# Performance work log

Measured on AMD Instinct MI355X. Metric: run time of the kernel, lower is better.

Reference implementation:

```python
import jax, jax.numpy as jnp
import numpy as np
from jax import lax

STRIDE = 2
PAD = 2
K = 5

def conv_transpose3d(x, w, b):
    # x: (N, Cin, D, H, W); w: (Cin, Cout, kD, kH, kW) torch layout
    # Equivalent dense conv: flip kernel spatially, swap in/out, lhs-dilate by stride,
    # pad each side by (K - 1 - PAD).
    w_t = jnp.flip(w, axis=(2, 3, 4)).transpose(1, 0, 2, 3, 4)  # (Cout, Cin, kD, kH, kW)
    p = K - 1 - PAD  # = 2
    y = lax.conv_general_dilated(
        x, w_t,
        window_strides=(1, 1, 1),
        padding=[(p, p)] * 3,
        lhs_dilation=(STRIDE,) * 3,
        dimension_numbers=('NCDHW', 'OIDHW', 'NCDHW'))
    return y + b[None, :, None, None, None]

def maxpool3d(x, k):
    return lax.reduce_window(
        x, -jnp.inf, lax.max,
        window_dimensions=(1, 1, k, k, k),
        window_strides=(1, 1, k, k, k),
        padding='VALID')

def setup_inputs() -> dict:
    key = jax.random.key(0)
    k1, k2, k3 = jax.random.split(key, 3)
    x = jax.random.normal(k1, (16, 32, 16, 32, 32), dtype=jnp.float32)
    weight = jax.random.normal(k2, (32, 64, 5, 5, 5), dtype=jnp.float32) * 0.05
    bias = jax.random.normal(k3, (64,), dtype=jnp.float32) * 0.05
    return {"x": x, "weight": weight, "bias": bias}

def reference(x, weight, bias):
    y = conv_transpose3d(x, weight, bias)      # (16, 64, 31, 63, 63)
    y = maxpool3d(y, 2)                        # (16, 64, 15, 31, 31)
    y = maxpool3d(y, 3)                        # (16, 64, 5, 10, 10)
    return jnp.sum(y, axis=1, keepdims=True)   # (16, 1, 5, 10, 10)
```

## Files before the change

### kernel.cpp

```cpp
#include <hip/hip_runtime.h>

typedef short v8s __attribute__((ext_vector_type(8)));
typedef float v4f __attribute__((ext_vector_type(4)));

#define N_  16
#define CI_ 32
#define CO_ 64
#define DI  16
#define HI  32
#define WI  32
#define NEGINF (-__builtin_inff())

__device__ __forceinline__ unsigned short f2bf(float f) {
    unsigned int u = __float_as_uint(f);
    unsigned int r = (u + 0x7FFFu + ((u >> 16) & 1u)) >> 16;
    return (unsigned short)r;
}

__device__ __forceinline__ void gld16(const void* g, void* l) {
    __builtin_amdgcn_global_load_lds(
        (const __attribute__((address_space(1))) void*)g,
        (__attribute__((address_space(3))) void*)l, 16, 0, 0);
}

__constant__ int O64c[9] = {0, 55296, 92160, 129024, 153600, 190464, 215040, 239616, 256000};

__global__ void prep(const float* __restrict__ x, const float* __restrict__ w,
                     unsigned short* __restrict__ xp, unsigned short* __restrict__ wt,
                     float* __restrict__ out, int do_x) {
    if (blockIdx.x < 1088) {
        if (!do_x) return;
        __shared__ __align__(16) unsigned short tl[8192];
        const int bi = blockIdx.x;
        const int pd = bi % 17;
        const int cg = (bi / 17) & 3;
        const int n  = bi / 68;
        if (pd > 0) {
            const int c = threadIdx.x >> 5;
            const int ww = threadIdx.x & 31;
            const float* xc = x + (((size_t)(n * 32 + cg * 8 + c) * 16 + (pd - 1)) * 32) * 32;
            #pragma unroll
            for (int h = 0; h < 32; ++h)
                tl[(h * 32 + ww) * 8 + c] = f2bf(xc[h * 32 + ww]);
        }
        __syncthreads();
        unsigned short* xpo = xp + (size_t)bi * 8448;
        for (int o = threadIdx.x; o < 1056; o += 256) {
            int ph = o / 33, pw = o - ph * 33;
            v8s v;
            if (pd == 0 || ph == 0 || pw == 0) v = (v8s){0, 0, 0, 0, 0, 0, 0, 0};
            else v = *(const v8s*)&tl[((ph - 1) * 32 + pw - 1) * 8];
            *(v8s*)(xpo + o * 8) = v;
        }
    } else {
        if (blockIdx.x == 1088 && threadIdx.x < 64) {
            int tb = 1536 + threadIdx.x;
            int whalf = tb & 1, hj = (tb >> 1) % 10, dj = (tb / 20) % 5, n = tb / 100;
            float* o = out + (((size_t)(n * 5 + dj) * 10 + hj) * 10 + whalf * 5);
            #pragma unroll
            for (int j = 0; j < 5; ++j) o[j] = 0.f;
        }
        int u = (blockIdx.x - 1088) * 256 + threadIdx.x;
        if (u >= 256000) return;
        int r = 0;
        #pragma unroll
        for (int i = 1; i < 8; ++i) r += (u >= O64c[i]);
        const int rd = r >> 2, rh = (r >> 1) & 1, rw = r & 1;
        const int nh = rh ? 2 : 3, nw = rw ? 2 : 3;
        int t2 = u - O64c[r];
        int j   = t2 & 7;
        int l   = (t2 >> 3) & 15;
        int q   = (t2 >> 7) & 3;
        int nt  = (t2 >> 9) & 3;
        int tap = t2 >> 11;
        int co = nt * 16 + l;
        int ci = q * 8 + j;
        int jw = tap % nw;
        int jh = (tap / nw) % nh;
        int jd = tap / (nw * nh);
        int kd = rd + 2 * jd, kh = rh + 2 * jh, kw = rw + 2 * jw;
        wt[u] = f2bf(w[(ci * CO_ + co) * 125 + kd * 25 + kh * 5 + kw]);
    }
}

__device__ __forceinline__ void run_class_f(
        const unsigned short* __restrict__ xs,
        int laneAB,
        const unsigned short* __restrict__ wcls,
        const int taps, const int nw, const int nh,
        unsigned Bm, bool isQ3, float (&pmax)[4][2])
{
    const char* xb = (const char*)xs;

    v4f acc[9][4];
    #pragma unroll
    for (int t = 0; t < 9; ++t)
        #pragma unroll
        for (int nt = 0; nt < 4; ++nt)
            acc[t][nt] = (v4f){0.f, 0.f, 0.f, 0.f};

    v8s B0[4], B1[4];
    #pragma unroll
    for (int nt = 0; nt < 4; ++nt) B0[nt] = *(const v8s*)(wcls + nt * 512);

    int aoff = 0, jw = 0, jh = 0;
    auto adv = [&]() {
        aoff += 16; ++jw;
        if (jw == nw) { jw = 0; aoff += 288 - 16 * nw; ++jh;
            if (jh == nh) { jh = 0; aoff += 1440 - 288 * nh; } }
    };
    auto comp = [&](const v8s (&B)[4]) {
        const int va = laneAB - aoff;
        static constexpr int RO[9] = {0, 576, 1728, 2880, 3456, 288, 1440, 2016, 3168};
        #pragma unroll
        for (int rr = 0; rr < 9; ++rr) {
            v8s a = *(const v8s*)(xb + va + RO[rr]);
            #pragma unroll
            for (int nt = 0; nt < 4; ++nt)
                acc[rr][nt] = __builtin_amdgcn_mfma_f32_16x16x32_bf16(a, B[nt], acc[rr][nt], 0, 0, 0);
        }
    };

    int s = 0;
    while (s + 2 <= taps) {
        #pragma unroll
        for (int nt = 0; nt < 4; ++nt)
            B1[nt] = *(const v8s*)(wcls + ((s + 1) * 4 + nt) * 512);
        comp(B0); adv();
        if (s + 2 < taps) {
            #pragma unroll
            for (int nt = 0; nt < 4; ++nt)
                B0[nt] = *(const v8s*)(wcls + ((s + 2) * 4 + nt) * 512);
        }
        comp(B1); adv();
        s += 2;
    }
    if (s < taps) comp(B0);

    #pragma unroll
    for (int nt = 0; nt < 4; ++nt) {
        #pragma unroll
        for (int reg = 0; reg < 4; ++reg) {
            float v = acc[0][nt][reg];
            #pragma unroll
            for (int rr = 1; rr < 9; ++rr) v = fmaxf(v, acc[rr][nt][reg]);
            if (reg == 3) v = isQ3 ? NEGINF : v;
            const bool bB = (Bm >> reg) & 1u;
            pmax[nt][0] = fmaxf(pmax[nt][0], bB ? NEGINF : v);
            pmax[nt][1] = fmaxf(pmax[nt][1], bB ? v : NEGINF);
        }
    }
}

__device__ __forceinline__ void run_class_t(
        const unsigned short* __restrict__ xs,
        int laneAB,
        const unsigned short* __restrict__ wcls,
        const int taps, const int nw, const int nh,
        unsigned Bm, bool isQ3, float (&pmax)[2])
{
    const char* xb = (const char*)xs;

    v4f acc[9];
    #pragma unroll
    for (int t = 0; t < 9; ++t) acc[t] = (v4f){0.f, 0.f, 0.f, 0.f};

    v8s B0 = *(const v8s*)(wcls);
    v8s B1;

    int aoff = 0, jw = 0, jh = 0;
    auto adv = [&]() {
        aoff += 16; ++jw;
        if (jw == nw) { jw = 0; aoff += 288 - 16 * nw; ++jh;
            if (jh == nh) { jh = 0; aoff += 1440 - 288 * nh; } }
    };
    auto comp = [&](v8s B) {
        const int va = laneAB - aoff;
        static constexpr int RO[9] = {0, 576, 1728, 2880, 3456, 288, 1440, 2016, 3168};
        #pragma unroll
        for (int rr = 0; rr < 9; ++rr) {
            v8s a = *(const v8s*)(xb + va + RO[rr]);
            acc[rr] = __builtin_amdgcn_mfma_f32_16x16x32_bf16(a, B, acc[rr], 0, 0, 0);
        }
    };

    int s = 0;
    while (s + 2 <= taps) {
        B1 = *(const v8s*)(wcls + (s + 1) * 2048);
        comp(B0); adv();
        if (s + 2 < taps) B0 = *(const v8s*)(wcls + (s + 2) * 2048);
        comp(B1); adv();
        s += 2;
    }
    if (s < taps) comp(B0);

    #pragma unroll
    for (int reg = 0; reg < 4; ++reg) {
        float v = acc[0][reg];
        #pragma unroll
        for (int rr = 1; rr < 9; ++rr) v = fmaxf(v, acc[rr][reg]);
        if (reg == 3) v = isQ3 ? NEGINF : v;
        const bool bB = (Bm >> reg) & 1u;
        pmax[0] = fmaxf(pmax[0], bB ? NEGINF : v);
        pmax[1] = fmaxf(pmax[1], bB ? v : NEGINF);
    }
}

template<bool PRE>
__global__ __launch_bounds__(256, 2)
void fused_main(const float* __restrict__ x, const unsigned short* __restrict__ xp,
                const unsigned short* __restrict__ wt,
                const float* __restrict__ bias, float* __restrict__ out) {
    __shared__ __align__(16) char smem[28800];
    unsigned short* xs = (unsigned short*)smem;
    float* P = (float*)smem;
    float* Y = (float*)(smem + 9472);

    const int b = blockIdx.x;
    const bool tail = (b >= 1536);
    int tile, sub;
    if (tail) { int u = b - 1536; tile = 1536 + (u >> 2); sub = u & 3; }
    else      { tile = b; sub = 0; }

    const int whalf = tile & 1;
    const int hj = (tile >> 1) % 10;
    const int dj = (tile / 20) % 5;
    const int n  = tile / 100;

    const int lane = threadIdx.x & 63;
    const int wv   = threadIdx.x >> 6;

    if (PRE) {
        const int t = threadIdx.x;
        #pragma unroll
        for (int i = 0; i < 8; ++i) {
            int c = i * 256 + t;
            if (c < 1800) {
                int row = c / 18;
                int iwc = c - row * 18;
                int cg  = row / 25;
                int rr  = row - cg * 25;
                int idl = rr / 5;
                int ihl = rr - idl * 5;
                size_t goff = ((((size_t)((n * 4 + cg) * 17 + 3 * dj + idl)) * 32
                                + 3 * hj + ihl) * 33 + 15 * whalf + iwc) * 8;
                gld16(xp + goff, smem + i * 4096 + wv * 1024);
            }
        }
    } else {
        const int id0 = 3 * dj - 1, ih0 = 3 * hj - 1, iwb = 15 * whalf - 1;
        const float* xn = x + (size_t)n * (CI_ * DI * HI * WI);
        for (int e = threadIdx.x; e < 14400; e += 256) {
            int ci   = e / 450;
            int rem  = e - ci * 450;
            int idp  = rem / 90;
            int rem2 = rem - idp * 90;
            int ihp  = rem2 / 18;
            int iwp  = rem2 - ihp * 18;
            int id = id0 + idp, ih = ih0 + ihp, iw = iwb + iwp;
            float v = 0.f;
            if (id >= 0 && ih >= 0 && iw >= 0)
                v = xn[((ci * DI + id) * HI + ih) * WI + iw];
            xs[(ci >> 3) * 3600 + idp * 720 + ihp * 144 + iwp * 8 + (ci & 7)] = f2bf(v);
        }
    }
    __syncthreads();

    const int l = lane & 15, q = lane >> 4;
    const int laneAB = q * 7200 + (l + 2) * 16 + 3456;

    static constexpr int tapsT[8] = {27, 18, 18, 12, 18, 12, 12, 8};
    static constexpr int O64[8]   = {0, 55296, 92160, 129024, 153600, 190464, 215040, 239616};
    static constexpr int nwT[8]   = {3, 2, 3, 2, 3, 2, 3, 2};
    static constexpr int nhT[8]   = {3, 3, 2, 2, 3, 3, 2, 2};
    static constexpr int uOff[5] = {0, 2, 4, 6, 8};
    static constexpr int uR[8]   = {0, 7,  1, 3,  2, 5,  4, 6};

    static constexpr int wjAt[4] = {0, 1, 2, 4};
    static constexpr int wjBt[4] = {1, 2, 3, 5};

    const unsigned Bm = (0x0EC8u >> (q << 2)) & 0xFu;
    const bool isQ3 = (q == 3);
    const int u0 = uOff[wv], u1 = uOff[wv + 1];

    if (!tail) {
        float pmax[4][2];
        #pragma unroll
        for (int nt = 0; nt < 4; ++nt) { pmax[nt][0] = NEGINF; pmax[nt][1] = NEGINF; }

        #pragma unroll 1
        for (int iu = u0; iu < u1; ++iu) {
            const int r = uR[iu];
            run_class_f(xs, laneAB, wt + O64[r] + lane * 8,
                        tapsT[r], nwT[r], nhT[r], Bm, isQ3, pmax);
        }

        __syncthreads();
        {
            int base = ((wv * 4 + q) * 16 + l) * 9;
            #pragma unroll
            for (int nt = 0; nt < 4; ++nt) {
                P[base + nt * 2 + 0] = pmax[nt][0];
                P[base + nt * 2 + 1] = pmax[nt][1];
            }
        }
        __syncthreads();

        for (int oi = threadIdx.x; oi < 320; oi += 256) {
            int co = oi / 5;
            int wjl = oi - co * 5;
            int lc = co & 15, ntc = co >> 4;
            float v = NEGINF;
            #pragma unroll
            for (int w = 0; w < 4; ++w) {
                #pragma unroll
                for (int qq = 0; qq < 4; ++qq) {
                    const float* pp = &P[((w * 4 + qq) * 16 + lc) * 9 + ntc * 2];
                    if (wjAt[qq] == wjl) v = fmaxf(v, pp[0]);
                    if (wjBt[qq] == wjl) v = fmaxf(v, pp[1]);
                }
            }
            Y[co * 5 + wjl] = v + bias[co];
        }
        __syncthreads();

        if (wv == 0) {
            float vy[5];
            #pragma unroll
            for (int wjl = 0; wjl < 5; ++wjl) vy[wjl] = Y[lane * 5 + wjl];
            #pragma unroll
            for (int wjl = 0; wjl < 5; ++wjl) {
                float v = vy[wjl];
                #pragma unroll
                for (int off = 32; off > 0; off >>= 1)
                    v += __shfl_down(v, off, 64);
                if (lane == 0)
                    out[((n * 5 + dj) * 10 + hj) * 10 + whalf * 5 + wjl] = v;
            }
        }
    } else {
        float pmax1[2];
        pmax1[0] = NEGINF; pmax1[1] = NEGINF;

        #pragma unroll 1
        for (int iu = u0; iu < u1; ++iu) {
            const int r = uR[iu];
            run_class_t(xs, laneAB, wt + O64[r] + sub * 512 + lane * 8,
                        tapsT[r], nwT[r], nhT[r], Bm, isQ3, pmax1);
        }

        __syncthreads();
        {
            int base = ((wv * 4 + q) * 16 + l) * 9;
            P[base + sub * 2 + 0] = pmax1[0];
            P[base + sub * 2 + 1] = pmax1[1];
        }
        __syncthreads();

        if (wv == 0) {
            const int co = lane;
            const int lc = co & 15, ntc = co >> 4;
            const bool valid = (ntc == sub);
            float vy[5];
            #pragma unroll
            for (int wjl = 0; wjl < 5; ++wjl) vy[wjl] = NEGINF;
            #pragma unroll
            for (int w = 0; w < 4; ++w) {
                #pragma unroll
                for (int qq = 0; qq < 4; ++qq) {
                    const float* pp = &P[((w * 4 + qq) * 16 + lc) * 9 + sub * 2];
                    float a = pp[0], bv = pp[1];
                    #pragma unroll
                    for (int wjl = 0; wjl < 5; ++wjl) {
                        if (wjAt[qq] == wjl) vy[wjl] = fmaxf(vy[wjl], a);
                        if (wjBt[qq] == wjl) vy[wjl] = fmaxf(vy[wjl], bv);
                    }
                }
            }
            #pragma unroll
            for (int wjl = 0; wjl < 5; ++wjl) {
                float v = valid ? (vy[wjl] + bias[co]) : 0.f;
                #pragma unroll
                for (int off = 32; off > 0; off >>= 1)
                    v += __shfl_down(v, off, 64);
                if (lane == 0)
                    atomicAdd(&out[((n * 5 + dj) * 10 + hj) * 10 + whalf * 5 + wjl], v);
            }
        }
    }
}

extern "C" void kernel_launch(void* const* d_in, const int* in_sizes, int n_in,
                              void* d_out, int out_size, void* d_ws, size_t ws_size,
                              hipStream_t stream) {
    const float* x    = (const float*)d_in[0];
    const float* w    = (const float*)d_in[1];
    const float* bias = (const float*)d_in[2];
    float*       out  = (float*)d_out;
    unsigned short* wt = (unsigned short*)d_ws;
    unsigned short* xp = (unsigned short*)((char*)d_ws + 512512);
    const size_t XP_NEED = 512512 + 18382848;
    const int do_x = (ws_size >= XP_NEED) ? 1 : 0;

    prep<<<dim3(2088), 256, 0, stream>>>(x, w, xp, wt, out, do_x);
    if (do_x)
        fused_main<true ><<<dim3(1792), 256, 0, stream>>>(x, xp, wt, bias, out);
    else
        fused_main<false><<<dim3(1792), 256, 0, stream>>>(x, xp, wt, bias, out);
}
```

Before: 174.6 us.

## Merge prep and main kernels into one persistent cooperative kernel with grid sync

Replaces the two-launch sequence (prep then fused_main) with one cooperative kernel of 512 persistent blocks. The blocks first do the input/weight bf16 repacking, then pass a grid-wide barrier and loop over the conv/pool tiles. The aim is to remove the second launch and its inter-kernel gap. In exchange, the tile work is now scheduled statically: 3 full tiles per block plus a tail that lands on half the blocks, which leaves the load imbalanced. The tile body moves into a noinline device function, which may add call overhead or cost register allocation quality.

```diff
diff --git a/kernel.cpp b/kernel.cpp
--- a/kernel.cpp
+++ b/kernel.cpp
@@ -1,4 +1,5 @@
 #include <hip/hip_runtime.h>
+#include <hip/hip_cooperative_groups.h>
 
 typedef short v8s __attribute__((ext_vector_type(8)));
 typedef float v4f __attribute__((ext_vector_type(4)));
@@ -25,61 +26,74 @@
 
 __constant__ int O64c[9] = {0, 55296, 92160, 129024, 153600, 190464, 215040, 239616, 256000};
 
+
+__device__ __forceinline__ void xprep_block(int bi, const float* __restrict__ x,
+                                            unsigned short* __restrict__ xp,
+                                            unsigned short* tl) {
+    const int pd = bi % 17;
+    const int cg = (bi / 17) & 3;
+    const int n  = bi / 68;
+    if (pd > 0) {
+        const int c = threadIdx.x >> 5;
+        const int ww = threadIdx.x & 31;
+        const float* xc = x + (((size_t)(n * 32 + cg * 8 + c) * 16 + (pd - 1)) * 32) * 32;
+        #pragma unroll
+        for (int h = 0; h < 32; ++h)
+            tl[(h * 32 + ww) * 8 + c] = f2bf(xc[h * 32 + ww]);
+    }
+    __syncthreads();
+    unsigned short* xpo = xp + (size_t)bi * 8448;
+    for (int o = threadIdx.x; o < 1056; o += 256) {
+        int ph = o / 33, pw = o - ph * 33;
+        v8s v;
+        if (pd == 0 || ph == 0 || pw == 0) v = (v8s){0, 0, 0, 0, 0, 0, 0, 0};
+        else v = *(const v8s*)&tl[((ph - 1) * 32 + pw - 1) * 8];
+        *(v8s*)(xpo + o * 8) = v;
+    }
+}
+
+__device__ __forceinline__ void wprep_one(int u, const float* __restrict__ w,
+                                          unsigned short* __restrict__ wt) {
+    int r = 0;
+    #pragma unroll
+    for (int i = 1; i < 8; ++i) r += (u >= O64c[i]);
+    const int rd = r >> 2, rh = (r >> 1) & 1, rw = r & 1;
+    const int nh = rh ? 2 : 3, nw = rw ? 2 : 3;
+    int t2 = u - O64c[r];
+    int j   = t2 & 7;
+    int l   = (t2 >> 3) & 15;
+    int q   = (t2 >> 7) & 3;
+    int nt  = (t2 >> 9) & 3;
+    int tap = t2 >> 11;
+    int co = nt * 16 + l;
+    int ci = q * 8 + j;
+    int jw = tap % nw;
+    int jh = (tap / nw) % nh;
+    int jd = tap / (nw * nh);
+    int kd = rd + 2 * jd, kh = rh + 2 * jh, kw = rw + 2 * jw;
+    wt[u] = f2bf(w[(ci * CO_ + co) * 125 + kd * 25 + kh * 5 + kw]);
+}
+
+__device__ __forceinline__ void tailzero(float* __restrict__ out, int t) {
+    int tb = 1536 + t;
+    int whalf = tb & 1, hj = (tb >> 1) % 10, dj = (tb / 20) % 5, n = tb / 100;
+    float* o = out + (((size_t)(n * 5 + dj) * 10 + hj) * 10 + whalf * 5);
+    #pragma unroll
+    for (int j = 0; j < 5; ++j) o[j] = 0.f;
+}
+
 __global__ void prep(const float* __restrict__ x, const float* __restrict__ w,
                      unsigned short* __restrict__ xp, unsigned short* __restrict__ wt,
                      float* __restrict__ out, int do_x) {
     if (blockIdx.x < 1088) {
         if (!do_x) return;
         __shared__ __align__(16) unsigned short tl[8192];
-        const int bi = blockIdx.x;
-        const int pd = bi % 17;
-        const int cg = (bi / 17) & 3;
-        const int n  = bi / 68;
-        if (pd > 0) {
-            const int c = threadIdx.x >> 5;
-            const int ww = threadIdx.x & 31;
-            const float* xc = x + (((size_t)(n * 32 + cg * 8 + c) * 16 + (pd - 1)) * 32) * 32;
-            #pragma unroll
-            for (int h = 0; h < 32; ++h)
-                tl[(h * 32 + ww) * 8 + c] = f2bf(xc[h * 32 + ww]);
-        }
-        __syncthreads();
-        unsigned short* xpo = xp + (size_t)bi * 8448;
-        for (int o = threadIdx.x; o < 1056; o += 256) {
-            int ph = o / 33, pw = o - ph * 33;
-            v8s v;
-            if (pd == 0 || ph == 0 || pw == 0) v = (v8s){0, 0, 0, 0, 0, 0, 0, 0};
-            else v = *(const v8s*)&tl[((ph - 1) * 32 + pw - 1) * 8];
-            *(v8s*)(xpo + o * 8) = v;
-        }
+        xprep_block(blockIdx.x, x, xp, tl);
     } else {
-        if (blockIdx.x == 1088 && threadIdx.x < 64) {
-            int tb = 1536 + threadIdx.x;
-            int whalf = tb & 1, hj = (tb >> 1) % 10, dj = (tb / 20) % 5, n = tb / 100;
-            float* o = out + (((size_t)(n * 5 + dj) * 10 + hj) * 10 + whalf * 5);
-            #pragma unroll
-            for (int j = 0; j < 5; ++j) o[j] = 0.f;
-        }
+        if (blockIdx.x == 1088 && threadIdx.x < 64) tailzero(out, threadIdx.x);
         int u = (blockIdx.x - 1088) * 256 + threadIdx.x;
         if (u >= 256000) return;
-        int r = 0;
-        #pragma unroll
-        for (int i = 1; i < 8; ++i) r += (u >= O64c[i]);
-        const int rd = r >> 2, rh = (r >> 1) & 1, rw = r & 1;
-        const int nh = rh ? 2 : 3, nw = rw ? 2 : 3;
-        int t2 = u - O64c[r];
-        int j   = t2 & 7;
-        int l   = (t2 >> 3) & 15;
-        int q   = (t2 >> 7) & 3;
-        int nt  = (t2 >> 9) & 3;
-        int tap = t2 >> 11;
-        int co = nt * 16 + l;
-        int ci = q * 8 + j;
-        int jw = tap % nw;
-        int jh = (tap / nw) % nh;
-        int jd = tap / (nw * nh);
-        int kd = rd + 2 * jd, kh = rh + 2 * jh, kw = rw + 2 * jw;
-        wt[u] = f2bf(w[(ci * CO_ + co) * 125 + kd * 25 + kh * 5 + kw]);
+        wprep_one(u, w, wt);
     }
 }
 
@@ -207,20 +221,14 @@
 }
 
 template<bool PRE>
-__global__ __launch_bounds__(256, 2)
-void fused_main(const float* __restrict__ x, const unsigned short* __restrict__ xp,
-                const unsigned short* __restrict__ wt,
-                const float* __restrict__ bias, float* __restrict__ out) {
-    __shared__ __align__(16) char smem[28800];
+__device__ __attribute__((noinline)) void do_tile(
+        int tile, int sub, bool tail,
+        const float* __restrict__ x, const unsigned short* __restrict__ xp,
+        const unsigned short* __restrict__ wt, const float* __restrict__ bias,
+        float* __restrict__ out, char* smem) {
     unsigned short* xs = (unsigned short*)smem;
     float* P = (float*)smem;
     float* Y = (float*)(smem + 9472);
-
-    const int b = blockIdx.x;
-    const bool tail = (b >= 1536);
-    int tile, sub;
-    if (tail) { int u = b - 1536; tile = 1536 + (u >> 2); sub = u & 3; }
-    else      { tile = b; sub = 0; }
 
     const int whalf = tile & 1;
     const int hj = (tile >> 1) % 10;
@@ -388,6 +396,49 @@
             }
         }
     }
+    __syncthreads();
+}
+
+template<bool PRE>
+__global__ __launch_bounds__(256, 2)
+void fused_main(const float* __restrict__ x, const unsigned short* __restrict__ xp,
+                const unsigned short* __restrict__ wt,
+                const float* __restrict__ bias, float* __restrict__ out) {
+    __shared__ __align__(16) char smem[28800];
+    const int b = blockIdx.x;
+    const bool tail = (b >= 1536);
+    int tile, sub;
+    if (tail) { int u = b - 1536; tile = 1536 + (u >> 2); sub = u & 3; }
+    else      { tile = b; sub = 0; }
+    do_tile<PRE>(tile, sub, tail, x, xp, wt, bias, out, smem);
+}
+
+__global__ __launch_bounds__(256, 2)
+void mono(const float* __restrict__ x, const float* __restrict__ w,
+          const float* __restrict__ bias, unsigned short* __restrict__ xp,
+          unsigned short* __restrict__ wt, float* __restrict__ out) {
+    __shared__ __align__(16) char smem[28800];
+
+    #pragma unroll 1
+    for (int bi = blockIdx.x; bi < 1088; bi += 512) {
+        xprep_block(bi, x, xp, (unsigned short*)smem);
+        __syncthreads();
+    }
+    #pragma unroll 1
+    for (int u = blockIdx.x * 256 + threadIdx.x; u < 256000; u += 512 * 256)
+        wprep_one(u, w, wt);
+    if (blockIdx.x == 511 && threadIdx.x < 64) tailzero(out, threadIdx.x);
+
+    __threadfence();
+    cooperative_groups::this_grid().sync();
+
+    #pragma unroll 1
+    for (int rep = 0; rep < 3; ++rep)
+        do_tile<true>((int)blockIdx.x + rep * 512, 0, false, x, xp, wt, bias, out, smem);
+    if (blockIdx.x >= 256) {
+        int qb = blockIdx.x - 256;
+        do_tile<true>(1536 + (qb >> 2), qb & 3, true, x, xp, wt, bias, out, smem);
+    }
 }
 
 extern "C" void kernel_launch(void* const* d_in, const int* in_sizes, int n_in,
@@ -402,9 +453,17 @@
     const size_t XP_NEED = 512512 + 18382848;
     const int do_x = (ws_size >= XP_NEED) ? 1 : 0;
 
-    prep<<<dim3(2088), 256, 0, stream>>>(x, w, xp, wt, out, do_x);
-    if (do_x)
+    if (do_x) {
+        void* args[6] = {(void*)&x, (void*)&w, (void*)&bias,
+                         (void*)&xp, (void*)&wt, (void*)&out};
+        hipError_t e = hipLaunchCooperativeKernel((const void*)mono, dim3(512),
+                                                  dim3(256), args, 0, stream);
+        if (e == hipSuccess) return;
+        (void)hipGetLastError();
+        prep<<<dim3(2088), 256, 0, stream>>>(x, w, xp, wt, out, 1);
         fused_main<true ><<<dim3(1792), 256, 0, stream>>>(x, xp, wt, bias, out);
-    else
+    } else {
+        prep<<<dim3(2088), 256, 0, stream>>>(x, w, xp, wt, out, 0);
         fused_main<false><<<dim3(1792), 256, 0, stream>>>(x, xp, wt, bias, out);
-}
+    }
+}
```

Result: slower. 314.2 us (+79.9%).

## Split output-channel tiles into two halves to cut accumulator registers and raise occupancy

Applied to the files above, without the earlier changes.

The main conv-pool loop now processes the 64 output channels in two passes of 32 (two 16-wide MFMA tiles each) instead of all four tiles at once. This halves the accumulator array from 36 to 18 v4f registers, and the launch bound goes from 2 to 3 blocks per CU to exploit the lower register pressure. In exchange, every input A fragment is read from LDS twice per class, and the tap loop and pool reduction run twice, adding LDS traffic and loop overhead.

```diff
diff --git a/kernel.cpp b/kernel.cpp
--- a/kernel.cpp
+++ b/kernel.cpp
@@ -83,25 +83,28 @@
     }
 }
 
-__device__ __forceinline__ void run_class_f(
+__device__ __forceinline__ void run_class_h(
         const unsigned short* __restrict__ xs,
         int laneAB,
-        const unsigned short* __restrict__ wcls,
+        const unsigned short* __restrict__ wclsh,
         const int taps, const int nw, const int nh,
-        unsigned Bm, bool isQ3, float (&pmax)[4][2])
+        unsigned Bm, bool isQ3, float (&pm)[2][2])
 {
     const char* xb = (const char*)xs;
 
-    v4f acc[9][4];
+    v4f acc[9][2];
     #pragma unroll
-    for (int t = 0; t < 9; ++t)
-        #pragma unroll
-        for (int nt = 0; nt < 4; ++nt)
-            acc[t][nt] = (v4f){0.f, 0.f, 0.f, 0.f};
-
-    v8s B0[4], B1[4];
-    #pragma unroll
-    for (int nt = 0; nt < 4; ++nt) B0[nt] = *(const v8s*)(wcls + nt * 512);
+    for (int t = 0; t < 9; ++t) {
+        acc[t][0] = (v4f){0.f, 0.f, 0.f, 0.f};
+        acc[t][1] = (v4f){0.f, 0.f, 0.f, 0.f};
+    }
+
+    v8s P0[2], P1[2], P2[2], P3[2];
+    P0[0] = *(const v8s*)(wclsh + 0);
+    P0[1] = *(const v8s*)(wclsh + 512);
+    P1[0] = *(const v8s*)(wclsh + 2048);
+    P1[1] = *(const v8s*)(wclsh + 2048 + 512);
+    P2[0] = P0[0]; P2[1] = P0[1]; P3[0] = P1[0]; P3[1] = P1[1];
 
     int aoff = 0, jw = 0, jh = 0;
     auto adv = [&]() {
@@ -109,45 +112,46 @@
         if (jw == nw) { jw = 0; aoff += 288 - 16 * nw; ++jh;
             if (jh == nh) { jh = 0; aoff += 1440 - 288 * nh; } }
     };
-    auto comp = [&](const v8s (&B)[4]) {
+    auto comp = [&](const v8s (&B)[2]) {
         const int va = laneAB - aoff;
         static constexpr int RO[9] = {0, 576, 1728, 2880, 3456, 288, 1440, 2016, 3168};
         #pragma unroll
         for (int rr = 0; rr < 9; ++rr) {
             v8s a = *(const v8s*)(xb + va + RO[rr]);
-            #pragma unroll
-            for (int nt = 0; nt < 4; ++nt)
-                acc[rr][nt] = __builtin_amdgcn_mfma_f32_16x16x32_bf16(a, B[nt], acc[rr][nt], 0, 0, 0);
+            acc[rr][0] = __builtin_amdgcn_mfma_f32_16x16x32_bf16(a, B[0], acc[rr][0], 0, 0, 0);
+            acc[rr][1] = __builtin_amdgcn_mfma_f32_16x16x32_bf16(a, B[1], acc[rr][1], 0, 0, 0);
         }
     };
 
     int s = 0;
     while (s + 2 <= taps) {
-        #pragma unroll
-        for (int nt = 0; nt < 4; ++nt)
-            B1[nt] = *(const v8s*)(wcls + ((s + 1) * 4 + nt) * 512);
-        comp(B0); adv();
         if (s + 2 < taps) {
-            #pragma unroll
-            for (int nt = 0; nt < 4; ++nt)
-                B0[nt] = *(const v8s*)(wcls + ((s + 2) * 4 + nt) * 512);
-        }
-        comp(B1); adv();
+            P2[0] = *(const v8s*)(wclsh + (s + 2) * 2048);
+            P2[1] = *(const v8s*)(wclsh + (s + 2) * 2048 + 512);
+        }
+        if (s + 3 < taps) {
+            P3[0] = *(const v8s*)(wclsh + (s + 3) * 2048);
+            P3[1] = *(const v8s*)(wclsh + (s + 3) * 2048 + 512);
+        }
+        comp(P0); adv();
+        comp(P1); adv();
+        P0[0] = P2[0]; P0[1] = P2[1];
+        P1[0] = P3[0]; P1[1] = P3[1];
         s += 2;
     }
-    if (s < taps) comp(B0);
+    if (s < taps) comp(P0);
 
     #pragma unroll
-    for (int nt = 0; nt < 4; ++nt) {
+    for (int j = 0; j < 2; ++j) {
         #pragma unroll
         for (int reg = 0; reg < 4; ++reg) {
-            float v = acc[0][nt][reg];
-            #pragma unroll
-            for (int rr = 1; rr < 9; ++rr) v = fmaxf(v, acc[rr][nt][reg]);
+            float v = acc[0][j][reg];
+            #pragma unroll
+            for (int rr = 1; rr < 9; ++rr) v = fmaxf(v, acc[rr][j][reg]);
             if (reg == 3) v = isQ3 ? NEGINF : v;
             const bool bB = (Bm >> reg) & 1u;
-            pmax[nt][0] = fmaxf(pmax[nt][0], bB ? NEGINF : v);
-            pmax[nt][1] = fmaxf(pmax[nt][1], bB ? v : NEGINF);
+            pm[j][0] = fmaxf(pm[j][0], bB ? NEGINF : v);
+            pm[j][1] = fmaxf(pm[j][1], bB ? v : NEGINF);
         }
     }
 }
@@ -207,7 +211,7 @@
 }
 
 template<bool PRE>
-__global__ __launch_bounds__(256, 2)
+__global__ __launch_bounds__(256, 3)
 void fused_main(const float* __restrict__ x, const unsigned short* __restrict__ xp,
                 const unsigned short* __restrict__ wt,
                 const float* __restrict__ bias, float* __restrict__ out) {
@@ -291,8 +295,23 @@
         #pragma unroll 1
         for (int iu = u0; iu < u1; ++iu) {
             const int r = uR[iu];
-            run_class_f(xs, laneAB, wt + O64[r] + lane * 8,
-                        tapsT[r], nwT[r], nhT[r], Bm, isQ3, pmax);
+            #pragma unroll 1
+            for (int h = 0; h < 2; ++h) {
+                float pm[2][2] = {{NEGINF, NEGINF}, {NEGINF, NEGINF}};
+                run_class_h(xs, laneAB, wt + O64[r] + h * 1024 + lane * 8,
+                            tapsT[r], nwT[r], nhT[r], Bm, isQ3, pm);
+                if (h == 0) {
+                    pmax[0][0] = fmaxf(pmax[0][0], pm[0][0]);
+                    pmax[0][1] = fmaxf(pmax[0][1], pm[0][1]);
+                    pmax[1][0] = fmaxf(pmax[1][0], pm[1][0]);
+                    pmax[1][1] = fmaxf(pmax[1][1], pm[1][1]);
+                } else {
+                    pmax[2][0] = fmaxf(pmax[2][0], pm[0][0]);
+                    pmax[2][1] = fmaxf(pmax[2][1], pm[0][1]);
+                    pmax[3][0] = fmaxf(pmax[3][0], pm[1][0]);
+                    pmax[3][1] = fmaxf(pmax[3][1], pm[1][1]);
+                }
+            }
         }
 
         __syncthreads();
```

New measurement: 179.9 us. 1.03x slower.

## Switch conv MFMA tiles from 16x16x32 to 32x32x16 bf16 with repacked weights

Applied to the files above, without the earlier changes.

The implicit-GEMM convolution now uses 32x32x16 bf16 MFMA instead of 16x16x32. The weight prep packing, the A-operand addressing (two ci halves per lane group), the accumulator-to-pool masking and the LDS partial-max layout are all reworked to match the 32x32 output fragment. The aim is fewer MFMA issues and fewer LDS A-loads per tap. The tail blocks now split Cout into 2 halves instead of 4, giving a smaller grid, and setprio is raised around the MFMA bursts. Risks are higher register pressure from the 16-wide accumulators and subtle indexing errors in the remapped layouts.

```diff
diff --git a/kernel.cpp b/kernel.cpp
--- a/kernel.cpp
+++ b/kernel.cpp
@@ -1,7 +1,7 @@
 #include <hip/hip_runtime.h>
 
 typedef short v8s __attribute__((ext_vector_type(8)));
-typedef float v4f __attribute__((ext_vector_type(4)));
+typedef float v16f __attribute__((ext_vector_type(16)));
 
 #define N_  16
 #define CI_ 32
@@ -67,14 +67,14 @@
         for (int i = 1; i < 8; ++i) r += (u >= O64c[i]);
         const int rd = r >> 2, rh = (r >> 1) & 1, rw = r & 1;
         const int nh = rh ? 2 : 3, nw = rw ? 2 : 3;
-        int t2 = u - O64c[r];
-        int j   = t2 & 7;
-        int l   = (t2 >> 3) & 15;
-        int q   = (t2 >> 7) & 3;
-        int nt  = (t2 >> 9) & 3;
-        int tap = t2 >> 11;
-        int co = nt * 16 + l;
-        int ci = q * 8 + j;
+        int t2   = u - O64c[r];
+        int j    = t2 & 7;
+        int lane = (t2 >> 3) & 63;
+        int tile = (t2 >> 9) & 1;
+        int p    = (t2 >> 10) & 1;
+        int tap  = t2 >> 11;
+        int co = tile * 32 + (lane & 31);
+        int ci = p * 16 + (lane >> 5) * 8 + j;
         int jw = tap % nw;
         int jh = (tap / nw) % nh;
         int jd = tap / (nw * nh);
@@ -83,25 +83,28 @@
     }
 }
 
+__constant__ int RO2e[10] = {0, 576, 1728, 2880, 3456, 288, 1440, 2016, 3168, 3168};
+
 __device__ __forceinline__ void run_class_f(
         const unsigned short* __restrict__ xs,
-        int laneAB,
+        int baseP0, int baseP1,
+        const int (&ROl)[5],
         const unsigned short* __restrict__ wcls,
         const int taps, const int nw, const int nh,
-        unsigned Bm, bool isQ3, float (&pmax)[4][2])
+        unsigned Bm0, unsigned Bm1, bool hHi, float (&pmax)[2][2][2])
 {
     const char* xb = (const char*)xs;
 
-    v4f acc[9][4];
-    #pragma unroll
-    for (int t = 0; t < 9; ++t)
-        #pragma unroll
-        for (int nt = 0; nt < 4; ++nt)
-            acc[t][nt] = (v4f){0.f, 0.f, 0.f, 0.f};
+    v16f acc[5][2];
+    #pragma unroll
+    for (int pr = 0; pr < 5; ++pr) {
+        acc[pr][0] = (v16f)0.f;
+        acc[pr][1] = (v16f)0.f;
+    }
 
     v8s B0[4], B1[4];
     #pragma unroll
-    for (int nt = 0; nt < 4; ++nt) B0[nt] = *(const v8s*)(wcls + nt * 512);
+    for (int f = 0; f < 4; ++f) B0[f] = *(const v8s*)(wcls + f * 512);
 
     int aoff = 0, jw = 0, jh = 0;
     auto adv = [&]() {
@@ -110,63 +113,74 @@
             if (jh == nh) { jh = 0; aoff += 1440 - 288 * nh; } }
     };
     auto comp = [&](const v8s (&B)[4]) {
-        const int va = laneAB - aoff;
-        static constexpr int RO[9] = {0, 576, 1728, 2880, 3456, 288, 1440, 2016, 3168};
-        #pragma unroll
-        for (int rr = 0; rr < 9; ++rr) {
-            v8s a = *(const v8s*)(xb + va + RO[rr]);
-            #pragma unroll
-            for (int nt = 0; nt < 4; ++nt)
-                acc[rr][nt] = __builtin_amdgcn_mfma_f32_16x16x32_bf16(a, B[nt], acc[rr][nt], 0, 0, 0);
-        }
+        __builtin_amdgcn_s_setprio(1);
+        #pragma unroll
+        for (int pr = 0; pr < 5; ++pr) {
+            v8s a0 = *(const v8s*)(xb + baseP0 + ROl[pr] - aoff);
+            v8s a1 = *(const v8s*)(xb + baseP1 + ROl[pr] - aoff);
+            acc[pr][0] = __builtin_amdgcn_mfma_f32_32x32x16_bf16(a0, B[0], acc[pr][0], 0, 0, 0);
+            acc[pr][1] = __builtin_amdgcn_mfma_f32_32x32x16_bf16(a0, B[1], acc[pr][1], 0, 0, 0);
+            acc[pr][0] = __builtin_amdgcn_mfma_f32_32x32x16_bf16(a1, B[2], acc[pr][0], 0, 0, 0);
+            acc[pr][1] = __builtin_amdgcn_mfma_f32_32x32x16_bf16(a1, B[3], acc[pr][1], 0, 0, 0);
+        }
+        __builtin_amdgcn_s_setprio(0);
+    };
+    auto ldB = [&](v8s (&B)[4], int t) {
+        #pragma unroll
+        for (int f = 0; f < 4; ++f)
+            B[f] = *(const v8s*)(wcls + t * 2048 + f * 512);
     };
 
     int s = 0;
     while (s + 2 <= taps) {
-        #pragma unroll
-        for (int nt = 0; nt < 4; ++nt)
-            B1[nt] = *(const v8s*)(wcls + ((s + 1) * 4 + nt) * 512);
+        ldB(B1, s + 1);
         comp(B0); adv();
-        if (s + 2 < taps) {
-            #pragma unroll
-            for (int nt = 0; nt < 4; ++nt)
-                B0[nt] = *(const v8s*)(wcls + ((s + 2) * 4 + nt) * 512);
-        }
+        if (s + 2 < taps) ldB(B0, s + 2);
         comp(B1); adv();
         s += 2;
     }
     if (s < taps) comp(B0);
 
     #pragma unroll
-    for (int nt = 0; nt < 4; ++nt) {
-        #pragma unroll
-        for (int reg = 0; reg < 4; ++reg) {
-            float v = acc[0][nt][reg];
-            #pragma unroll
-            for (int rr = 1; rr < 9; ++rr) v = fmaxf(v, acc[rr][nt][reg]);
-            if (reg == 3) v = isQ3 ? NEGINF : v;
-            const bool bB = (Bm >> reg) & 1u;
-            pmax[nt][0] = fmaxf(pmax[nt][0], bB ? NEGINF : v);
-            pmax[nt][1] = fmaxf(pmax[nt][1], bB ? v : NEGINF);
+    for (int tl = 0; tl < 2; ++tl) {
+        #pragma unroll
+        for (int reg = 0; reg < 16; ++reg) {
+            float v = acc[0][tl][reg];
+            #pragma unroll
+            for (int pr = 1; pr < 5; ++pr) v = fmaxf(v, acc[pr][tl][reg]);
+            const int qi = (reg >> 2) & 1;
+            const int regm = reg & 3;
+            if (hHi && qi == 1 && regm == 3) v = NEGINF;
+            const unsigned bm = qi ? Bm1 : Bm0;
+            const bool bB = (bm >> regm) & 1u;
+            if (qi == 0) {
+                pmax[tl][0][0] = fmaxf(pmax[tl][0][0], bB ? NEGINF : v);
+                pmax[tl][0][1] = fmaxf(pmax[tl][0][1], bB ? v : NEGINF);
+            } else {
+                pmax[tl][1][0] = fmaxf(pmax[tl][1][0], bB ? NEGINF : v);
+                pmax[tl][1][1] = fmaxf(pmax[tl][1][1], bB ? v : NEGINF);
+            }
         }
     }
 }
 
 __device__ __forceinline__ void run_class_t(
         const unsigned short* __restrict__ xs,
-        int laneAB,
+        int baseP0, int baseP1,
+        const int (&ROl)[5],
         const unsigned short* __restrict__ wcls,
         const int taps, const int nw, const int nh,
-        unsigned Bm, bool isQ3, float (&pmax)[2])
+        unsigned Bm0, unsigned Bm1, bool hHi, float (&pm)[2][2])
 {
     const char* xb = (const char*)xs;
 
-    v4f acc[9];
-    #pragma unroll
-    for (int t = 0; t < 9; ++t) acc[t] = (v4f){0.f, 0.f, 0.f, 0.f};
-
-    v8s B0 = *(const v8s*)(wcls);
-    v8s B1;
+    v16f acc[5];
+    #pragma unroll
+    for (int pr = 0; pr < 5; ++pr) acc[pr] = (v16f)0.f;
+
+    v8s B0[2], B1[2];
+    B0[0] = *(const v8s*)(wcls + 0);
+    B0[1] = *(const v8s*)(wcls + 1024);
 
     int aoff = 0, jw = 0, jh = 0;
     auto adv = [&]() {
@@ -174,35 +188,47 @@
         if (jw == nw) { jw = 0; aoff += 288 - 16 * nw; ++jh;
             if (jh == nh) { jh = 0; aoff += 1440 - 288 * nh; } }
     };
-    auto comp = [&](v8s B) {
-        const int va = laneAB - aoff;
-        static constexpr int RO[9] = {0, 576, 1728, 2880, 3456, 288, 1440, 2016, 3168};
-        #pragma unroll
-        for (int rr = 0; rr < 9; ++rr) {
-            v8s a = *(const v8s*)(xb + va + RO[rr]);
-            acc[rr] = __builtin_amdgcn_mfma_f32_16x16x32_bf16(a, B, acc[rr], 0, 0, 0);
-        }
+    auto comp = [&](const v8s (&B)[2]) {
+        #pragma unroll
+        for (int pr = 0; pr < 5; ++pr) {
+            v8s a0 = *(const v8s*)(xb + baseP0 + ROl[pr] - aoff);
+            v8s a1 = *(const v8s*)(xb + baseP1 + ROl[pr] - aoff);
+            acc[pr] = __builtin_amdgcn_mfma_f32_32x32x16_bf16(a0, B[0], acc[pr], 0, 0, 0);
+            acc[pr] = __builtin_amdgcn_mfma_f32_32x32x16_bf16(a1, B[1], acc[pr], 0, 0, 0);
+        }
+    };
+    auto ldB = [&](v8s (&B)[2], int t) {
+        B[0] = *(const v8s*)(wcls + t * 2048 + 0);
+        B[1] = *(const v8s*)(wcls + t * 2048 + 1024);
     };
 
     int s = 0;
     while (s + 2 <= taps) {
-        B1 = *(const v8s*)(wcls + (s + 1) * 2048);
+        ldB(B1, s + 1);
         comp(B0); adv();
-        if (s + 2 < taps) B0 = *(const v8s*)(wcls + (s + 2) * 2048);
+        if (s + 2 < taps) ldB(B0, s + 2);
         comp(B1); adv();
         s += 2;
     }
     if (s < taps) comp(B0);
 
     #pragma unroll
-    for (int reg = 0; reg < 4; ++reg) {
+    for (int reg = 0; reg < 16; ++reg) {
         float v = acc[0][reg];
         #pragma unroll
-        for (int rr = 1; rr < 9; ++rr) v = fmaxf(v, acc[rr][reg]);
-        if (reg == 3) v = isQ3 ? NEGINF : v;
-        const bool bB = (Bm >> reg) & 1u;
-        pmax[0] = fmaxf(pmax[0], bB ? NEGINF : v);
-        pmax[1] = fmaxf(pmax[1], bB ? v : NEGINF);
+        for (int pr = 1; pr < 5; ++pr) v = fmaxf(v, acc[pr][reg]);
+        const int qi = (reg >> 2) & 1;
+        const int regm = reg & 3;
+        if (hHi && qi == 1 && regm == 3) v = NEGINF;
+        const unsigned bm = qi ? Bm1 : Bm0;
+        const bool bB = (bm >> regm) & 1u;
+        if (qi == 0) {
+            pm[0][0] = fmaxf(pm[0][0], bB ? NEGINF : v);
+            pm[0][1] = fmaxf(pm[0][1], bB ? v : NEGINF);
+        } else {
+            pm[1][0] = fmaxf(pm[1][0], bB ? NEGINF : v);
+            pm[1][1] = fmaxf(pm[1][1], bB ? v : NEGINF);
+        }
     }
 }
 
@@ -219,7 +245,7 @@
     const int b = blockIdx.x;
     const bool tail = (b >= 1536);
     int tile, sub;
-    if (tail) { int u = b - 1536; tile = 1536 + (u >> 2); sub = u & 3; }
+    if (tail) { int u = b - 1536; tile = 1536 + (u >> 1); sub = u & 1; }
     else      { tile = b; sub = 0; }
 
     const int whalf = tile & 1;
@@ -266,8 +292,19 @@
     }
     __syncthreads();
 
-    const int l = lane & 15, q = lane >> 4;
-    const int laneAB = q * 7200 + (l + 2) * 16 + 3456;
+    const int h    = lane >> 5;
+    const int r32  = lane & 31;
+    const int hi   = r32 >> 4;
+    const int mrow = r32 & 15;
+    const int baseP0 = (0 + h) * 7200 + (mrow + 2) * 16 + 3456;
+    const int baseP1 = (2 + h) * 7200 + (mrow + 2) * 16 + 3456;
+    int ROl[5];
+    #pragma unroll
+    for (int pr = 0; pr < 5; ++pr) ROl[pr] = RO2e[pr * 2 + hi];
+
+    const unsigned Bm0 = (0x0EC8u >> (h * 4)) & 0xFu;
+    const unsigned Bm1 = (0x0EC8u >> ((h + 2) * 4)) & 0xFu;
+    const bool hHi = (h == 1);
 
     static constexpr int tapsT[8] = {27, 18, 18, 12, 18, 12, 12, 8};
     static constexpr int O64[8]   = {0, 55296, 92160, 129024, 153600, 190464, 215040, 239616};
@@ -279,29 +316,32 @@
     static constexpr int wjAt[4] = {0, 1, 2, 4};
     static constexpr int wjBt[4] = {1, 2, 3, 5};
 
-    const unsigned Bm = (0x0EC8u >> (q << 2)) & 0xFu;
-    const bool isQ3 = (q == 3);
     const int u0 = uOff[wv], u1 = uOff[wv + 1];
 
     if (!tail) {
-        float pmax[4][2];
-        #pragma unroll
-        for (int nt = 0; nt < 4; ++nt) { pmax[nt][0] = NEGINF; pmax[nt][1] = NEGINF; }
+        float pmax[2][2][2];
+        #pragma unroll
+        for (int tl = 0; tl < 2; ++tl)
+            #pragma unroll
+            for (int qi = 0; qi < 2; ++qi) { pmax[tl][qi][0] = NEGINF; pmax[tl][qi][1] = NEGINF; }
 
         #pragma unroll 1
         for (int iu = u0; iu < u1; ++iu) {
             const int r = uR[iu];
-            run_class_f(xs, laneAB, wt + O64[r] + lane * 8,
-                        tapsT[r], nwT[r], nhT[r], Bm, isQ3, pmax);
-        }
-
-        __syncthreads();
-        {
-            int base = ((wv * 4 + q) * 16 + l) * 9;
-            #pragma unroll
-            for (int nt = 0; nt < 4; ++nt) {
-                P[base + nt * 2 + 0] = pmax[nt][0];
-                P[base + nt * 2 + 1] = pmax[nt][1];
+            run_class_f(xs, baseP0, baseP1, ROl, wt + O64[r] + lane * 8,
+                        tapsT[r], nwT[r], nhT[r], Bm0, Bm1, hHi, pmax);
+        }
+
+        __syncthreads();
+        #pragma unroll
+        for (int tl = 0; tl < 2; ++tl) {
+            #pragma unroll
+            for (int qi = 0; qi < 2; ++qi) {
+                const int q = h + 2 * qi;
+                const int co = tl * 32 + r32;
+                const int idx = ((wv * 4 + q) * 64 + co) * 2;
+                P[idx + 0] = pmax[tl][qi][0];
+                P[idx + 1] = pmax[tl][qi][1];
             }
         }
         __syncthreads();
@@ -309,13 +349,12 @@
         for (int oi = threadIdx.x; oi < 320; oi += 256) {
             int co = oi / 5;
             int wjl = oi - co * 5;
-            int lc = co & 15, ntc = co >> 4;
             float v = NEGINF;
             #pragma unroll
             for (int w = 0; w < 4; ++w) {
                 #pragma unroll
                 for (int qq = 0; qq < 4; ++qq) {
-                    const float* pp = &P[((w * 4 + qq) * 16 + lc) * 9 + ntc * 2];
+                    const float* pp = &P[((w * 4 + qq) * 64 + co) * 2];
                     if (wjAt[qq] == wjl) v = fmaxf(v, pp[0]);
                     if (wjBt[qq] == wjl) v = fmaxf(v, pp[1]);
                 }
@@ -339,28 +378,30 @@
             }
         }
     } else {
-        float pmax1[2];
-        pmax1[0] = NEGINF; pmax1[1] = NEGINF;
+        float pm[2][2];
+        pm[0][0] = NEGINF; pm[0][1] = NEGINF;
+        pm[1][0] = NEGINF; pm[1][1] = NEGINF;
 
         #pragma unroll 1
         for (int iu = u0; iu < u1; ++iu) {
             const int r = uR[iu];
-            run_class_t(xs, laneAB, wt + O64[r] + sub * 512 + lane * 8,
-                        tapsT[r], nwT[r], nhT[r], Bm, isQ3, pmax1);
-        }
-
-        __syncthreads();
-        {
-            int base = ((wv * 4 + q) * 16 + l) * 9;
-            P[base + sub * 2 + 0] = pmax1[0];
-            P[base + sub * 2 + 1] = pmax1[1];
+            run_class_t(xs, baseP0, baseP1, ROl, wt + O64[r] + sub * 512 + lane * 8,
+                        tapsT[r], nwT[r], nhT[r], Bm0, Bm1, hHi, pm);
+        }
+
+        __syncthreads();
+        #pragma unroll
+        for (int qi = 0; qi < 2; ++qi) {
+            const int q = h + 2 * qi;
+            const int idx = ((wv * 4 + q) * 32 + r32) * 2;
+            P[idx + 0] = pm[qi][0];
+            P[idx + 1] = pm[qi][1];
         }
         __syncthreads();
 
         if (wv == 0) {
-            const int co = lane;
-            const int lc = co & 15, ntc = co >> 4;
-            const bool valid = (ntc == sub);
+            const bool valid = (lane < 32);
+            const int cl = lane & 31;
             float vy[5];
             #pragma unroll
             for (int wjl = 0; wjl < 5; ++wjl) vy[wjl] = NEGINF;
@@ -368,7 +409,7 @@
             for (int w = 0; w < 4; ++w) {
                 #pragma unroll
                 for (int qq = 0; qq < 4; ++qq) {
-                    const float* pp = &P[((w * 4 + qq) * 16 + lc) * 9 + sub * 2];
+                    const float* pp = &P[((w * 4 + qq) * 32 + cl) * 2];
                     float a = pp[0], bv = pp[1];
                     #pragma unroll
                     for (int wjl = 0; wjl < 5; ++wjl) {
@@ -379,7 +420,7 @@
             }
             #pragma unroll
             for (int wjl = 0; wjl < 5; ++wjl) {
-                float v = valid ? (vy[wjl] + bias[co]) : 0.f;
+                float v = valid ? (vy[wjl] + bias[sub * 32 + cl]) : 0.f;
                 #pragma unroll
                 for (int off = 32; off > 0; off >>= 1)
                     v += __shfl_down(v, off, 64);
@@ -404,7 +445,7 @@
 
     prep<<<dim3(2088), 256, 0, stream>>>(x, w, xp, wt, out, do_x);
     if (do_x)
-        fused_main<true ><<<dim3(1792), 256, 0, stream>>>(x, xp, wt, bias, out);
+        fused_main<true ><<<dim3(1664), 256, 0, stream>>>(x, xp, wt, bias, out);
     else
-        fused_main<false><<<dim3(1792), 256, 0, stream>>>(x, xp, wt, bias, out);
-}
+        fused_main<false><<<dim3(1664), 256, 0, stream>>>(x, xp, wt, bias, out);
+}
```

Result: slower. 192.2 us (+10.1%).
